# Optimization experiments

Measured on AMD Instinct MI355X. Metric: run time of the kernel, lower is better.

The kernel has to match this reference:

```python
import jax, jax.numpy as jnp
import numpy as np

B, S, H = 2, 1024, 2048
NH, HD = 16, 128
PAST = 1024
ROPE_THETA = 10000.0


def _rope(q, k, theta=ROPE_THETA):
    # q, k: [B, S, NH, HD]; standard rotate-half RoPE over current positions 0..S-1
    s, d = q.shape[1], q.shape[3]
    inv_freq = 1.0 / (theta ** (jnp.arange(0, d, 2, dtype=jnp.float32) / d))  # [d/2]
    freqs = jnp.arange(s, dtype=jnp.float32)[:, None] * inv_freq[None, :]      # [S, d/2]
    emb = jnp.concatenate([freqs, freqs], axis=-1)                             # [S, d]
    cos = jnp.cos(emb)[None, :, None, :]
    sin = jnp.sin(emb)[None, :, None, :]

    def rot_half(x):
        x1, x2 = jnp.split(x, 2, axis=-1)
        return jnp.concatenate([-x2, x1], axis=-1)

    return q * cos + rot_half(q) * sin, k * cos + rot_half(k) * sin


def setup_inputs() -> dict:
    key = jax.random.key(0)
    ks = jax.random.split(key, 12)
    hidden_states = jax.random.normal(ks[0], (B, S, H), dtype=jnp.float32)
    past_key = jax.random.normal(ks[1], (B, NH, PAST, HD), dtype=jnp.float32)
    past_value = jax.random.normal(ks[2], (B, NH, PAST, HD), dtype=jnp.float32)
    # causal mask accounting for cache: 1.0 where masked (query i cannot see kv j > PAST+i)
    q_pos = PAST + jnp.arange(S)[:, None]
    kv_pos = jnp.arange(PAST + S)[None, :]
    mask = jnp.broadcast_to((kv_pos > q_pos).astype(jnp.float32)[None, None], (B, 1, S, PAST + S))
    sc = 1.0 / np.sqrt(H)
    Wq = jax.random.normal(ks[3], (H, NH * HD), dtype=jnp.float32) * sc
    Wk = jax.random.normal(ks[4], (H, NH * HD), dtype=jnp.float32) * sc
    Wv = jax.random.normal(ks[5], (H, NH * HD), dtype=jnp.float32) * sc
    Wo = jax.random.normal(ks[6], (NH * HD, H), dtype=jnp.float32) * (1.0 / np.sqrt(NH * HD))
    bq = jnp.zeros((NH * HD,), jnp.float32)
    bk = jnp.zeros((NH * HD,), jnp.float32)
    bv = jnp.zeros((NH * HD,), jnp.float32)
    bo = jnp.zeros((H,), jnp.float32)
    return {"hidden_states": hidden_states, "mask": mask, "past_key": past_key,
            "past_value": past_value, "Wq": Wq, "bq": bq, "Wk": Wk, "bk": bk,
            "Wv": Wv, "bv": bv, "Wo": Wo, "bo": bo}


def reference(hidden_states, mask, past_key, past_value, Wq, bq, Wk, bk, Wv, bv, Wo, bo):
    b, s, _ = hidden_states.shape
    scale = 1.0 / jnp.sqrt(jnp.float32(HD))
    q = (hidden_states @ Wq + bq).reshape(b, s, NH, HD)
    k = (hidden_states @ Wk + bk).reshape(b, s, NH, HD)
    v = (hidden_states @ Wv + bv).reshape(b, s, NH, HD)
    q, k = _rope(q, k)
    q, k, v = (jnp.transpose(x, (0, 2, 1, 3)) for x in (q, k, v))  # [B,NH,S,HD]
    k = jnp.concatenate([past_key, k], axis=2)    # [B,NH,S_total,HD]
    v = jnp.concatenate([past_value, v], axis=2)
    scores = jnp.einsum('bhqd,bhkd->bhqk', q, k) * scale
    scores = scores + mask * (-1e9)               # mask broadcasts over heads
    probs = jax.nn.softmax(scores, axis=-1).astype(jnp.float32)
    out = jnp.einsum('bhqk,bhkd->bhqd', probs, v)
    out = out.transpose(0, 2, 1, 3).reshape(b, s, NH * HD)
    return out @ Wo + bo, k, v
```

## Files before the change

### kernel.cpp

```cpp
#include <hip/hip_runtime.h>
#include <hip/hip_bf16.h>
#include <math.h>

#define NB 2
#define SEQ 1024
#define HDIM 2048
#define NHEADS 16
#define HDHEAD 128
#define PASTN 1024
#define STOT 2048
#define MROWS 2048

typedef __attribute__((ext_vector_type(4))) float f32x4;
typedef __attribute__((ext_vector_type(8))) __bf16 bf16x8;
typedef __attribute__((ext_vector_type(8))) unsigned short us8;
typedef __attribute__((ext_vector_type(4))) unsigned short us4;

__device__ __forceinline__ unsigned short f2bf(float f) {
    union { float f; unsigned int u; } v; v.f = f;
    unsigned int u = v.u;
    u += 0x7FFFu + ((u >> 16) & 1u);
    return (unsigned short)(u >> 16);
}
__device__ __forceinline__ bf16x8 as_bf(us8 u) { return __builtin_bit_cast(bf16x8, u); }

__device__ __forceinline__ void gl16(const unsigned short* g, unsigned short* l) {
    __builtin_amdgcn_global_load_lds(
        (const __attribute__((address_space(1))) void*)g,
        (__attribute__((address_space(3))) void*)l, 16, 0, 0);
}

#define OFF_CS  ((size_t)0)
#define OFF_HSB (OFF_CS  + (size_t)SEQ*64*8)
#define OFF_WT  (OFF_HSB + (size_t)MROWS*HDIM*2)
#define OFF_QBF (OFF_WT  + (size_t)4*HDIM*HDIM*2)
#define OFF_KC  (OFF_QBF + (size_t)NB*NHEADS*SEQ*HDHEAD*2)
#define OFF_VT  (OFF_KC  + (size_t)NB*NHEADS*STOT*HDHEAD*2)
#define OFF_ATT (OFF_VT  + (size_t)NB*NHEADS*HDHEAD*STOT*2)


__global__ void k_prep(const float* __restrict__ in, unsigned short* __restrict__ hsb,
                       const float* __restrict__ pk, float* __restrict__ outK,
                       unsigned short* __restrict__ Kc2, float2* __restrict__ csT,
                       const float* __restrict__ Wq, const float* __restrict__ Wk,
                       const float* __restrict__ Wv, const float* __restrict__ Wo,
                       unsigned short* __restrict__ WT,
                       const float* __restrict__ pv, float* __restrict__ outV,
                       unsigned short* __restrict__ Vt2) {
    __shared__ unsigned short tsh[64][65];
    const int bid = blockIdx.x, tid = threadIdx.x;
    if (bid < 4096) {
        const int i = (bid * 256 + tid) * 4;
        {
            f32x4 v = *(const f32x4*)(in + i);
            us4 o;
            o.x = f2bf(v.x); o.y = f2bf(v.y); o.z = f2bf(v.z); o.w = f2bf(v.w);
            *(us4*)(hsb + i) = o;
        }
        {
            size_t e = (size_t)i;
            size_t bh = e >> 17;
            int p = (int)((e >> 7) & 1023);
            int d0 = (int)(e & 127);
            f32x4 v = *(const f32x4*)(pk + e);
            *(f32x4*)(outK + e + (bh << 17)) = v;
            us4 u;
            u.x = f2bf(v.x); u.y = f2bf(v.y); u.z = f2bf(v.z); u.w = f2bf(v.w);
            const int kt = p >> 6, pr = p & 63;
            *(us4*)(Kc2 + ((bh * 32 + kt) << 13) + (size_t)pr * 128 + (d0 ^ ((p & 7) << 3))) = u;
        }
        if (bid < 256) {
            const int idx = bid * 256 + tid;
            const int s = idx >> 6, fi = idx & 63;
            float inv = 1.0f / powf(10000.0f, (float)fi / 64.0f);
            float a = (float)s * inv;
            csT[idx] = make_float2(cosf(a), sinf(a));
        }
    } else if (bid < 8192) {
        const int idx = bid - 4096;
        const int z = idx >> 10;
        const int rem = idx & 1023;
        const int n0 = (rem & 31) * 64, k0 = (rem >> 5) * 64;
        const float* W = (z == 0) ? Wq : (z == 1) ? Wk : (z == 2) ? Wv : Wo;
        unsigned short* out = WT + (size_t)z * HDIM * HDIM;
        const int tx = tid & 63, ty = tid >> 6;
        #pragma unroll
        for (int j = 0; j < 16; ++j) {
            const int kk = ty + j * 4;
            tsh[tx][kk] = f2bf(W[(size_t)(k0 + kk) * HDIM + n0 + tx]);
        }
        __syncthreads();
        #pragma unroll
        for (int j = 0; j < 16; ++j) {
            const int nn = ty + j * 4;
            out[(size_t)(n0 + nn) * HDIM + k0 + tx] = tsh[nn][tx];
        }
    } else {
        const int idx = bid - 8192;
        const int bh = idx >> 5;
        const int rem = idx & 31;
        const int p0 = (rem & 15) * 64, d0 = (rem >> 4) * 64;
        const int tx = tid & 63, ty = tid >> 6;
        const float* src = pv + ((size_t)bh * PASTN + p0) * HDHEAD + d0;
        float* dst = outV + ((size_t)bh * STOT + p0) * HDHEAD + d0;
        #pragma unroll
        for (int j = 0; j < 16; ++j) {
            const int pp = ty + j * 4;
            float v = src[(size_t)pp * HDHEAD + tx];
            dst[(size_t)pp * HDHEAD + tx] = v;
            tsh[tx][pp] = f2bf(v);
        }
        __syncthreads();
        unsigned short* vt = Vt2 + (((size_t)bh * 32 + (p0 >> 6)) << 13);
        #pragma unroll
        for (int j = 0; j < 16; ++j) {
            const int dd = ty + j * 4;
            const int d = d0 + dd;
            vt[(size_t)d * 64 + (tx ^ ((d & 7) << 3))] = tsh[dd][tx];
        }
    }
}

__global__ __launch_bounds__(512, 2) void k_gemm_qkv(
    const unsigned short* __restrict__ hsb, const unsigned short* __restrict__ WT,
    const float* __restrict__ bq, const float* __restrict__ bk, const float* __restrict__ bv,
    const float2* __restrict__ csT,
    unsigned short* __restrict__ qbf, unsigned short* __restrict__ Kc2,
    unsigned short* __restrict__ Vt2, float* __restrict__ outK, float* __restrict__ outV) {
    __shared__ __align__(16) unsigned short As[2][256 * 64];
    __shared__ __align__(16) unsigned short Bs[2][256 * 64];

    const int bid = blockIdx.x;
    const int swz = (bid & 7) * 24 + (bid >> 3);
    const int mb = swz & 7;
    const int nbz = swz >> 3;
    const int z = nbz >> 3;
    const int nb8 = nbz & 7;
    const int m0 = mb * 256;
    const int n0 = nb8 * 256;
    const unsigned short* Wz = WT + (size_t)z * HDIM * HDIM;
    const float* bias = (z == 0) ? bq : (z == 1) ? bk : bv;

    const int t = threadIdx.x;
    const int lane = t & 63, wid = t >> 6;
    const int wr = wid >> 1, wc = wid & 1;
    const int c = lane & 15, g = lane >> 4;

    const int lrow8 = lane >> 3;
    const int lslot = (lane & 7) ^ lrow8;
    const unsigned short* aB = hsb + (size_t)(m0 + lrow8) * HDIM + lslot * 8;
    const unsigned short* bB = Wz + (size_t)(n0 + lrow8) * HDIM + lslot * 8;

    auto stage = [&](int kt, int pb) {
        const int k0s = kt * 64;
        #pragma unroll
        for (int j = 0; j < 4; ++j) {
            const int ch = wid * 4 + j;
            gl16(aB + (size_t)(ch * 8) * HDIM + k0s, &As[pb][ch * 512]);
            gl16(bB + (size_t)(ch * 8) * HDIM + k0s, &Bs[pb][ch * 512]);
        }
    };

    f32x4 acc[4][8] = {};
    const int NT = HDIM / 64;

    stage(0, 0);
    stage(1, 1);

    for (int kt = 0; kt < NT; ++kt) {
        const int p = kt & 1;
        if (kt + 1 < NT) {
            asm volatile("s_waitcnt vmcnt(8)" ::: "memory");
        } else {
            asm volatile("s_waitcnt vmcnt(0)" ::: "memory");
        }
        __builtin_amdgcn_s_barrier();
        bf16x8 bfr[8][2];
        #pragma unroll
        for (int ni = 0; ni < 8; ++ni) {
            const int br = wc * 128 + ni * 16 + c;
            const int sw = br & 7;
            bfr[ni][0] = as_bf(*(const us8*)&Bs[p][br * 64 + ((g ^ sw) << 3)]);
            bfr[ni][1] = as_bf(*(const us8*)&Bs[p][br * 64 + (((4 + g) ^ sw) << 3)]);
        }
        #pragma unroll
        for (int mi = 0; mi < 4; ++mi) {
            const int ar = wr * 64 + mi * 16 + c;
            const int swa = ar & 7;
            const bf16x8 a0 = as_bf(*(const us8*)&As[p][ar * 64 + ((g ^ swa) << 3)]);
            const bf16x8 a1 = as_bf(*(const us8*)&As[p][ar * 64 + (((4 + g) ^ swa) << 3)]);
            __builtin_amdgcn_s_setprio(1);
            #pragma unroll
            for (int ni = 0; ni < 8; ++ni)
                acc[mi][ni] = __builtin_amdgcn_mfma_f32_16x16x32_bf16(a0, bfr[ni][0], acc[mi][ni], 0, 0, 0);
            #pragma unroll
            for (int ni = 0; ni < 8; ++ni)
                acc[mi][ni] = __builtin_amdgcn_mfma_f32_16x16x32_bf16(a1, bfr[ni][1], acc[mi][ni], 0, 0, 0);
            __builtin_amdgcn_s_setprio(0);
            __builtin_amdgcn_s_barrier();
        }
        if (kt + 2 < NT) stage(kt + 2, p);
    }

    const float qscale = 0.08838834764831845f * 1.44269504088896f;
    const int h = nb8 * 2 + wc;
    #pragma unroll
    for (int mi = 0; mi < 4; ++mi) {
        #pragma unroll
        for (int r = 0; r < 4; ++r) {
            const int row = m0 + wr * 64 + mi * 16 + g * 4 + r;
            const int b = row >> 10, s = row & 1023;
            const size_t bh2 = (size_t)(b * NHEADS + h);
            const int p = PASTN + s;
            #pragma unroll
            for (int ni = 0; ni < 8; ++ni) {
                const int d = ni * 16 + c;
                const int nglob = n0 + wc * 128 + d;
                const float val = acc[mi][ni][r] + bias[nglob];
                if (z == 2) {
                    outV[(bh2 * STOT + p) * HDHEAD + d] = val;
                    Vt2[((bh2 * 32 + (p >> 6)) << 13) + (size_t)d * 64 +
                        ((p & 63) ^ ((d & 7) << 3))] = f2bf(val);
                } else {
                    const int fidx = d & 63;
                    const float2 cs = csT[s * 64 + fidx];
                    const float other = acc[mi][ni ^ 4][r] + bias[nglob ^ 64];
                    const float rot = (d < 64) ? (val * cs.x - other * cs.y)
                                               : (val * cs.x + other * cs.y);
                    if (z == 0) {
                        qbf[(bh2 * SEQ + s) * HDHEAD + d] = f2bf(rot * qscale);
                    } else {
                        Kc2[((bh2 * 32 + (p >> 6)) << 13) + (size_t)(p & 63) * 128 +
                            (d ^ ((p & 7) << 3))] = f2bf(rot);
                        outK[(bh2 * STOT + p) * HDHEAD + d] = rot;
                    }
                }
            }
        }
    }
}

__global__ __launch_bounds__(512) void k_attn(
    const unsigned short* __restrict__ qbf, const unsigned short* __restrict__ Kc2,
    const unsigned short* __restrict__ Vt2, unsigned short* __restrict__ attn) {
    __shared__ __align__(16) unsigned short Ks[2][64 * 128];
    __shared__ __align__(16) unsigned short Vs[128 * 64];
    __shared__ __align__(16) unsigned short P[8][16][72];
    const int qt = blockIdx.x;
    const int bh = blockIdx.y;
    const int b = bh >> 4, h = bh & 15;
    const int t = threadIdx.x, lane = t & 63, w = t >> 6;
    const int c = lane & 15, g = lane >> 4;
    const int q0 = qt * 128 + w * 16;
    const unsigned short* Qb = qbf + ((size_t)bh * SEQ + q0) * HDHEAD;
    const unsigned short* Kbase = Kc2 + ((size_t)bh << 18);
    const unsigned short* Vbase = Vt2 + ((size_t)bh << 18);

    bf16x8 qf[4];
    #pragma unroll
    for (int kf = 0; kf < 4; ++kf)
        qf[kf] = as_bf(*(const us8*)(Qb + (size_t)c * HDHEAD + kf * 32 + g * 8));

    #pragma unroll
    for (int j = 0; j < 2; ++j) {
        const int ch = w * 2 + j;
        gl16(Kbase + ch * 512 + lane * 8, &Ks[0][ch * 512]);
    }

    f32x4 o[8] = {};
    float mrow[4] = {-1e30f, -1e30f, -1e30f, -1e30f};
    float lrow[4] = {0.f, 0.f, 0.f, 0.f};
    const int nkt = 18 + 2 * qt;
    int cur = 0;
    for (int kt = 0; kt < nkt; ++kt) {
        asm volatile("s_waitcnt vmcnt(0)" ::: "memory");
        __builtin_amdgcn_s_barrier();
        const unsigned short* Vg = Vbase + ((size_t)kt << 13);
        #pragma unroll
        for (int j = 0; j < 2; ++j) {
            const int ch = w * 2 + j;
            gl16(Vg + ch * 512 + lane * 8, &Vs[ch * 512]);
        }
        if (kt + 1 < nkt) {
            const unsigned short* Kg = Kbase + ((size_t)(kt + 1) << 13);
            #pragma unroll
            for (int j = 0; j < 2; ++j) {
                const int ch = w * 2 + j;
                gl16(Kg + ch * 512 + lane * 8, &Ks[cur ^ 1][ch * 512]);
            }
        }
        f32x4 sa[4] = {};
        #pragma unroll
        for (int nf = 0; nf < 4; ++nf) {
            const int row = nf * 16 + c;
            const int swzr = (row & 7) << 3;
            #pragma unroll
            for (int kf = 0; kf < 4; ++kf) {
                bf16x8 kf8 = as_bf(*(const us8*)&Ks[cur][row * 128 + ((kf * 32 + g * 8) ^ swzr)]);
                sa[nf] = __builtin_amdgcn_mfma_f32_16x16x32_bf16(qf[kf], kf8, sa[nf], 0, 0, 0);
            }
        }
        const int k0 = kt * 64;
        if (k0 + 63 > PASTN + q0) {
            #pragma unroll
            for (int nf = 0; nf < 4; ++nf) {
                const int j = k0 + nf * 16 + c;
                #pragma unroll
                for (int r = 0; r < 4; ++r)
                    if (j > PASTN + q0 + g * 4 + r) sa[nf][r] = -1e30f;
            }
        }
        float pmax[4];
        #pragma unroll
        for (int r = 0; r < 4; ++r)
            pmax[r] = fmaxf(fmaxf(sa[0][r], sa[1][r]), fmaxf(sa[2][r], sa[3][r]));
        bool need = false;
        #pragma unroll
        for (int r = 0; r < 4; ++r) need = need || (pmax[r] > mrow[r] + 12.0f);
        if (__any(need)) {
            #pragma unroll
            for (int r = 0; r < 4; ++r) {
                float mx = pmax[r];
                mx = fmaxf(mx, __shfl_xor(mx, 1));
                mx = fmaxf(mx, __shfl_xor(mx, 2));
                mx = fmaxf(mx, __shfl_xor(mx, 4));
                mx = fmaxf(mx, __shfl_xor(mx, 8));
                const float mnew = fmaxf(mrow[r], mx);
                const float alpha = exp2f(mrow[r] - mnew);
                mrow[r] = mnew;
                lrow[r] *= alpha;
                #pragma unroll
                for (int nd = 0; nd < 8; ++nd) o[nd][r] *= alpha;
            }
        }
        #pragma unroll
        for (int r = 0; r < 4; ++r) {
            const float p0 = exp2f(sa[0][r] - mrow[r]);
            const float p1 = exp2f(sa[1][r] - mrow[r]);
            const float p2 = exp2f(sa[2][r] - mrow[r]);
            const float p3 = exp2f(sa[3][r] - mrow[r]);
            lrow[r] += (p0 + p1) + (p2 + p3);
            P[w][g * 4 + r][0 * 16 + c] = f2bf(p0);
            P[w][g * 4 + r][1 * 16 + c] = f2bf(p1);
            P[w][g * 4 + r][2 * 16 + c] = f2bf(p2);
            P[w][g * 4 + r][3 * 16 + c] = f2bf(p3);
        }
        if (kt + 1 < nkt) {
            asm volatile("s_waitcnt vmcnt(2)" ::: "memory");
        } else {
            asm volatile("s_waitcnt vmcnt(0)" ::: "memory");
        }
        __builtin_amdgcn_s_barrier();
        #pragma unroll
        for (int kf2 = 0; kf2 < 2; ++kf2) {
            const bf16x8 pa = as_bf(*(const us8*)&P[w][c][kf2 * 32 + g * 8]);
            #pragma unroll
            for (int nd = 0; nd < 8; ++nd) {
                const int d = nd * 16 + c;
                const bf16x8 vf = as_bf(*(const us8*)&Vs[d * 64 + ((kf2 * 32 + g * 8) ^ ((d & 7) << 3))]);
                o[nd] = __builtin_amdgcn_mfma_f32_16x16x32_bf16(pa, vf, o[nd], 0, 0, 0);
            }
        }
        cur ^= 1;
    }
    #pragma unroll
    for (int r = 0; r < 4; ++r) {
        float ls = lrow[r];
        ls += __shfl_xor(ls, 1);
        ls += __shfl_xor(ls, 2);
        ls += __shfl_xor(ls, 4);
        ls += __shfl_xor(ls, 8);
        const float inv = 1.0f / ls;
        #pragma unroll
        for (int nd = 0; nd < 8; ++nd) o[nd][r] *= inv;
    }
    #pragma unroll
    for (int nd = 0; nd < 8; ++nd)
        #pragma unroll
        for (int r = 0; r < 4; ++r) {
            const int srow = q0 + g * 4 + r;
            attn[((size_t)b * SEQ + srow) * HDIM + h * HDHEAD + nd * 16 + c] = f2bf(o[nd][r]);
        }
}

__global__ __launch_bounds__(256) void k_gemm_out(
    const unsigned short* __restrict__ attn, const unsigned short* __restrict__ WTo,
    const float* __restrict__ bo, float* __restrict__ out) {
    __shared__ __align__(16) unsigned char SMEM[65536];
    unsigned short* As0 = (unsigned short*)SMEM;
    unsigned short* Bs0 = (unsigned short*)(SMEM + 32768);
    const int m0 = blockIdx.y * 128;
    const int n0 = blockIdx.x * 128;
    const int t = threadIdx.x;
    const int lane = t & 63, w = t >> 6;
    const int c = lane & 15, g = lane >> 4;

    const int lrow = lane >> 3;
    const int lslot = (lane & 7) ^ lrow;
    const unsigned short* aB = attn + (size_t)(m0 + lrow) * HDIM + lslot * 8;
    const unsigned short* bB = WTo + (size_t)(n0 + lrow) * HDIM + lslot * 8;

    f32x4 acc[2][8] = {};
    const int NT = HDIM / 64;

    #pragma unroll
    for (int j = 0; j < 4; ++j) {
        const int ch = w * 4 + j;
        gl16(aB + (size_t)(ch * 8) * HDIM, &As0[ch * 512]);
        gl16(bB + (size_t)(ch * 8) * HDIM, &Bs0[ch * 512]);
    }
    for (int kt = 0; kt < NT; ++kt) {
        const int cb = kt & 1;
        if (kt + 1 < NT) {
            const int k1 = (kt + 1) * 64;
            #pragma unroll
            for (int j = 0; j < 4; ++j) {
                const int ch = w * 4 + j;
                gl16(aB + (size_t)(ch * 8) * HDIM + k1, &As0[(cb ^ 1) * 8192 + ch * 512]);
                gl16(bB + (size_t)(ch * 8) * HDIM + k1, &Bs0[(cb ^ 1) * 8192 + ch * 512]);
            }
            asm volatile("s_waitcnt vmcnt(8)" ::: "memory");
        } else {
            asm volatile("s_waitcnt vmcnt(0)" ::: "memory");
        }
        __builtin_amdgcn_s_barrier();
        #pragma unroll
        for (int kc = 0; kc < 2; ++kc) {
            bf16x8 af[2];
            #pragma unroll
            for (int mi = 0; mi < 2; ++mi) {
                const int ar = w * 32 + mi * 16 + c;
                af[mi] = as_bf(*(const us8*)&As0[cb * 8192 + ar * 64 + (((kc * 4 + g) ^ (ar & 7)) << 3)]);
            }
            #pragma unroll
            for (int ni = 0; ni < 8; ++ni) {
                const int br = ni * 16 + c;
                bf16x8 bfrag = as_bf(*(const us8*)&Bs0[cb * 8192 + br * 64 + (((kc * 4 + g) ^ (br & 7)) << 3)]);
                acc[0][ni] = __builtin_amdgcn_mfma_f32_16x16x32_bf16(af[0], bfrag, acc[0][ni], 0, 0, 0);
                acc[1][ni] = __builtin_amdgcn_mfma_f32_16x16x32_bf16(af[1], bfrag, acc[1][ni], 0, 0, 0);
            }
        }
        __builtin_amdgcn_s_barrier();
    }

    float* myF = (float*)SMEM + w * (16 * 132);
    const int qrow = lane & 31;
    for (int mi = 0; mi < 2; ++mi) {
        __syncthreads();
        #pragma unroll
        for (int r = 0; r < 4; ++r) {
            const int row = g * 4 + r;
            #pragma unroll
            for (int ni = 0; ni < 8; ++ni)
                myF[row * 132 + ni * 16 + c] = acc[mi][ni][r];
        }
        __syncthreads();
        #pragma unroll
        for (int j = 0; j < 8; ++j) {
            const int rrow = 2 * j + (lane >> 5);
            const int row = m0 + w * 32 + mi * 16 + rrow;
            f32x4 v4 = *(const f32x4*)&myF[rrow * 132 + qrow * 4];
            const f32x4 b4 = *(const f32x4*)&bo[n0 + qrow * 4];
            v4 += b4;
            *(f32x4*)&out[(size_t)row * HDIM + n0 + qrow * 4] = v4;
        }
    }
}

extern "C" void kernel_launch(void* const* d_in, const int* in_sizes, int n_in,
                              void* d_out, int out_size, void* d_ws, size_t ws_size,
                              hipStream_t stream) {
    const float* hidden = (const float*)d_in[0];
    const float* past_key = (const float*)d_in[2];
    const float* past_value = (const float*)d_in[3];
    const float* Wq = (const float*)d_in[4];
    const float* bq = (const float*)d_in[5];
    const float* Wk = (const float*)d_in[6];
    const float* bk = (const float*)d_in[7];
    const float* Wv = (const float*)d_in[8];
    const float* bv = (const float*)d_in[9];
    const float* Wo = (const float*)d_in[10];
    const float* bo = (const float*)d_in[11];

    float* out0 = (float*)d_out;
    float* outK = out0 + (size_t)NB * SEQ * HDIM;
    float* outV = outK + (size_t)NB * NHEADS * STOT * HDHEAD;

    char* ws = (char*)d_ws;
    float2* csT = (float2*)(ws + OFF_CS);
    unsigned short* hsb = (unsigned short*)(ws + OFF_HSB);
    unsigned short* WT = (unsigned short*)(ws + OFF_WT);
    unsigned short* qbf = (unsigned short*)(ws + OFF_QBF);
    unsigned short* Kc2 = (unsigned short*)(ws + OFF_KC);
    unsigned short* Vt2 = (unsigned short*)(ws + OFF_VT);
    unsigned short* attnb = (unsigned short*)(ws + OFF_ATT);

    k_prep<<<dim3(9216), dim3(256), 0, stream>>>(
        hidden, hsb, past_key, outK, Kc2, csT,
        Wq, Wk, Wv, Wo, WT, past_value, outV, Vt2);
    k_gemm_qkv<<<dim3(192), dim3(512), 0, stream>>>(
        hsb, WT, bq, bk, bv, csT, qbf, Kc2, Vt2, outK, outV);
    k_attn<<<dim3(8, 32), dim3(512), 0, stream>>>(qbf, Kc2, Vt2, attnb);
    k_gemm_out<<<dim3(16, 16), dim3(256), 0, stream>>>(
        attnb, WT + (size_t)3 * HDIM * HDIM, bo, out0);
}
```

Measured before the change: 234.3 us.

## Stage QKV GEMM epilogue through LDS for vectorized stores; split MFMA loop into phases

The QKV projection kernel's epilogue now writes each 16-row slice of results into per-warp shared-memory scratch, then reads it back so that Q, K, V, the fp32 cache outputs and the transposed V tile are written with 4-wide vector stores instead of scattered scalar stores. The main loop is also reorganised into four phases: all A fragments are loaded once, each phase loads two B column fragments, and an explicit lgkmcnt wait plus sched_barrier fences the MFMA block. The intent is to cut uncoalesced global write traffic and lower register pressure from holding all B fragments. The cost is extra __syncthreads in the epilogue, LDS round trips, and more barriers per k-step.

```diff
diff --git a/kernel.cpp b/kernel.cpp
--- a/kernel.cpp
+++ b/kernel.cpp
@@ -127,8 +127,9 @@
     const float2* __restrict__ csT,
     unsigned short* __restrict__ qbf, unsigned short* __restrict__ Kc2,
     unsigned short* __restrict__ Vt2, float* __restrict__ outK, float* __restrict__ outV) {
-    __shared__ __align__(16) unsigned short As[2][256 * 64];
-    __shared__ __align__(16) unsigned short Bs[2][256 * 64];
+    __shared__ __align__(16) unsigned char SMEM[131072];
+    unsigned short* As = (unsigned short*)SMEM;
+    unsigned short* Bs = (unsigned short*)(SMEM + 65536);
 
     const int bid = blockIdx.x;
     const int swz = (bid & 7) * 24 + (bid >> 3);
@@ -156,8 +157,8 @@
         #pragma unroll
         for (int j = 0; j < 4; ++j) {
             const int ch = wid * 4 + j;
-            gl16(aB + (size_t)(ch * 8) * HDIM + k0s, &As[pb][ch * 512]);
-            gl16(bB + (size_t)(ch * 8) * HDIM + k0s, &Bs[pb][ch * 512]);
+            gl16(aB + (size_t)(ch * 8) * HDIM + k0s, &As[pb * 16384 + ch * 512]);
+            gl16(bB + (size_t)(ch * 8) * HDIM + k0s, &Bs[pb * 16384 + ch * 512]);
         }
     };
 
@@ -175,66 +176,113 @@
             asm volatile("s_waitcnt vmcnt(0)" ::: "memory");
         }
         __builtin_amdgcn_s_barrier();
-        bf16x8 bfr[8][2];
-        #pragma unroll
-        for (int ni = 0; ni < 8; ++ni) {
-            const int br = wc * 128 + ni * 16 + c;
-            const int sw = br & 7;
-            bfr[ni][0] = as_bf(*(const us8*)&Bs[p][br * 64 + ((g ^ sw) << 3)]);
-            bfr[ni][1] = as_bf(*(const us8*)&Bs[p][br * 64 + (((4 + g) ^ sw) << 3)]);
-        }
-        #pragma unroll
-        for (int mi = 0; mi < 4; ++mi) {
-            const int ar = wr * 64 + mi * 16 + c;
-            const int swa = ar & 7;
-            const bf16x8 a0 = as_bf(*(const us8*)&As[p][ar * 64 + ((g ^ swa) << 3)]);
-            const bf16x8 a1 = as_bf(*(const us8*)&As[p][ar * 64 + (((4 + g) ^ swa) << 3)]);
+        bf16x8 a0[4], a1[4];
+        #pragma unroll
+        for (int ph = 0; ph < 4; ++ph) {
+            if (ph == 0) {
+                #pragma unroll
+                for (int mi = 0; mi < 4; ++mi) {
+                    const int ar = wr * 64 + mi * 16 + c;
+                    const int swa = ar & 7;
+                    a0[mi] = as_bf(*(const us8*)&As[p * 16384 + ar * 64 + ((g ^ swa) << 3)]);
+                    a1[mi] = as_bf(*(const us8*)&As[p * 16384 + ar * 64 + (((4 + g) ^ swa) << 3)]);
+                }
+            }
+            bf16x8 b0[2], b1[2];
+            #pragma unroll
+            for (int nj = 0; nj < 2; ++nj) {
+                const int br = wc * 128 + (ph * 2 + nj) * 16 + c;
+                const int sw = br & 7;
+                b0[nj] = as_bf(*(const us8*)&Bs[p * 16384 + br * 64 + ((g ^ sw) << 3)]);
+                b1[nj] = as_bf(*(const us8*)&Bs[p * 16384 + br * 64 + (((4 + g) ^ sw) << 3)]);
+            }
+            __builtin_amdgcn_s_barrier();
+            asm volatile("s_waitcnt lgkmcnt(0)" ::: "memory");
+            __builtin_amdgcn_sched_barrier(0);
             __builtin_amdgcn_s_setprio(1);
             #pragma unroll
-            for (int ni = 0; ni < 8; ++ni)
-                acc[mi][ni] = __builtin_amdgcn_mfma_f32_16x16x32_bf16(a0, bfr[ni][0], acc[mi][ni], 0, 0, 0);
-            #pragma unroll
-            for (int ni = 0; ni < 8; ++ni)
-                acc[mi][ni] = __builtin_amdgcn_mfma_f32_16x16x32_bf16(a1, bfr[ni][1], acc[mi][ni], 0, 0, 0);
+            for (int mi = 0; mi < 4; ++mi) {
+                #pragma unroll
+                for (int nj = 0; nj < 2; ++nj) {
+                    const int ni = ph * 2 + nj;
+                    acc[mi][ni] = __builtin_amdgcn_mfma_f32_16x16x32_bf16(a0[mi], b0[nj], acc[mi][ni], 0, 0, 0);
+                    acc[mi][ni] = __builtin_amdgcn_mfma_f32_16x16x32_bf16(a1[mi], b1[nj], acc[mi][ni], 0, 0, 0);
+                }
+            }
             __builtin_amdgcn_s_setprio(0);
             __builtin_amdgcn_s_barrier();
         }
         if (kt + 2 < NT) stage(kt + 2, p);
     }
 
+    float* myF = (float*)SMEM + wid * (16 * 132);
     const float qscale = 0.08838834764831845f * 1.44269504088896f;
     const int h = nb8 * 2 + wc;
-    #pragma unroll
+    const int b = m0 >> 10;
+    const size_t bh2 = (size_t)(b * NHEADS + h);
+    const int qrow = lane & 31;
+
     for (int mi = 0; mi < 4; ++mi) {
+        __syncthreads();
+        const int s_base = m0 + wr * 64 + mi * 16 - (b << 10);
         #pragma unroll
         for (int r = 0; r < 4; ++r) {
-            const int row = m0 + wr * 64 + mi * 16 + g * 4 + r;
-            const int b = row >> 10, s = row & 1023;
-            const size_t bh2 = (size_t)(b * NHEADS + h);
-            const int p = PASTN + s;
+            const int row = g * 4 + r;
+            const int s = s_base + row;
             #pragma unroll
             for (int ni = 0; ni < 8; ++ni) {
                 const int d = ni * 16 + c;
                 const int nglob = n0 + wc * 128 + d;
                 const float val = acc[mi][ni][r] + bias[nglob];
+                float sv;
                 if (z == 2) {
-                    outV[(bh2 * STOT + p) * HDHEAD + d] = val;
-                    Vt2[((bh2 * 32 + (p >> 6)) << 13) + (size_t)d * 64 +
-                        ((p & 63) ^ ((d & 7) << 3))] = f2bf(val);
+                    sv = val;
                 } else {
-                    const int fidx = d & 63;
-                    const float2 cs = csT[s * 64 + fidx];
+                    const float2 cs = csT[s * 64 + (d & 63)];
                     const float other = acc[mi][ni ^ 4][r] + bias[nglob ^ 64];
-                    const float rot = (d < 64) ? (val * cs.x - other * cs.y)
-                                               : (val * cs.x + other * cs.y);
-                    if (z == 0) {
-                        qbf[(bh2 * SEQ + s) * HDHEAD + d] = f2bf(rot * qscale);
-                    } else {
-                        Kc2[((bh2 * 32 + (p >> 6)) << 13) + (size_t)(p & 63) * 128 +
-                            (d ^ ((p & 7) << 3))] = f2bf(rot);
-                        outK[(bh2 * STOT + p) * HDHEAD + d] = rot;
-                    }
+                    sv = (d < 64) ? (val * cs.x - other * cs.y)
+                                  : (val * cs.x + other * cs.y);
+                    if (z == 0) sv *= qscale;
                 }
+                myF[row * 132 + d] = sv;
+            }
+        }
+        __syncthreads();
+        #pragma unroll
+        for (int j = 0; j < 8; ++j) {
+            const int rrow = 2 * j + (lane >> 5);
+            const int s = s_base + rrow;
+            const int p = PASTN + s;
+            const f32x4 v4 = *(const f32x4*)&myF[rrow * 132 + qrow * 4];
+            if (z == 0) {
+                us4 u;
+                u.x = f2bf(v4.x); u.y = f2bf(v4.y); u.z = f2bf(v4.z); u.w = f2bf(v4.w);
+                *(us4*)&qbf[(bh2 * SEQ + s) * HDHEAD + qrow * 4] = u;
+            } else if (z == 1) {
+                *(f32x4*)&outK[(bh2 * STOT + p) * HDHEAD + qrow * 4] = v4;
+                us4 u;
+                u.x = f2bf(v4.x); u.y = f2bf(v4.y); u.z = f2bf(v4.z); u.w = f2bf(v4.w);
+                *(us4*)&Kc2[((bh2 * 32 + (p >> 6)) << 13) + (size_t)(p & 63) * 128 +
+                            ((qrow * 4) ^ ((p & 7) << 3))] = u;
+            } else {
+                *(f32x4*)&outV[(bh2 * STOT + p) * HDHEAD + qrow * 4] = v4;
+            }
+        }
+        if (z == 2) {
+            const int p_base = PASTN + s_base;
+            const int ktv = p_base >> 6;
+            const int psub = (lane >> 4) * 4;
+            const int pr0 = (p_base & 63) + psub;
+            unsigned short* vbaseo = Vt2 + ((bh2 * 32 + ktv) << 13);
+            #pragma unroll
+            for (int jj = 0; jj < 8; ++jj) {
+                const int d = jj * 16 + c;
+                us4 u;
+                u.x = f2bf(myF[(psub + 0) * 132 + d]);
+                u.y = f2bf(myF[(psub + 1) * 132 + d]);
+                u.z = f2bf(myF[(psub + 2) * 132 + d]);
+                u.w = f2bf(myF[(psub + 3) * 132 + d]);
+                *(us4*)&vbaseo[d * 64 + (pr0 ^ ((d & 7) << 3))] = u;
             }
         }
     }
```

Result: slower. 267.3 us (+14.1%).

## Split QKV GEMM epilogue into separate RoPE/convert/transpose post kernel

Applied to the files above, without the earlier changes.

The QKV GEMM now writes raw fp32 Q and K tiles to scratch buffers (reusing the output and attention workspace) and writes V with bias directly. A new k_post kernel adds bias, applies RoPE, converts to bf16, writes the swizzled K cache and the transposed V via shared memory, all with vectorized stores. This replaces the scattered, uncoalesced scalar stores in the GEMM epilogue. The cost is an extra kernel launch and an extra fp32 round trip through global memory for Q, K and V.

```diff
diff --git a/kernel.cpp b/kernel.cpp
--- a/kernel.cpp
+++ b/kernel.cpp
@@ -123,10 +123,8 @@
 
 __global__ __launch_bounds__(512, 2) void k_gemm_qkv(
     const unsigned short* __restrict__ hsb, const unsigned short* __restrict__ WT,
-    const float* __restrict__ bq, const float* __restrict__ bk, const float* __restrict__ bv,
-    const float2* __restrict__ csT,
-    unsigned short* __restrict__ qbf, unsigned short* __restrict__ Kc2,
-    unsigned short* __restrict__ Vt2, float* __restrict__ outK, float* __restrict__ outV) {
+    const float* __restrict__ bv,
+    float* __restrict__ Cq, float* __restrict__ Ck, float* __restrict__ outV) {
     __shared__ __align__(16) unsigned short As[2][256 * 64];
     __shared__ __align__(16) unsigned short Bs[2][256 * 64];
 
@@ -139,7 +137,6 @@
     const int m0 = mb * 256;
     const int n0 = nb8 * 256;
     const unsigned short* Wz = WT + (size_t)z * HDIM * HDIM;
-    const float* bias = (z == 0) ? bq : (z == 1) ? bk : bv;
 
     const int t = threadIdx.x;
     const int lane = t & 63, wid = t >> 6;
@@ -202,41 +199,132 @@
         if (kt + 2 < NT) stage(kt + 2, p);
     }
 
+    if (z < 2) {
+        float* Cz = (z == 0) ? Cq : Ck;
+        #pragma unroll
+        for (int mi = 0; mi < 4; ++mi) {
+            #pragma unroll
+            for (int r = 0; r < 4; ++r) {
+                const size_t row = (size_t)(m0 + wr * 64 + mi * 16 + g * 4 + r);
+                #pragma unroll
+                for (int ni = 0; ni < 8; ++ni)
+                    Cz[row * HDIM + n0 + wc * 128 + ni * 16 + c] = acc[mi][ni][r];
+            }
+        }
+    } else {
+        const int h = nb8 * 2 + wc;
+        const int b = m0 >> 10;
+        const size_t bh2 = (size_t)(b * NHEADS + h);
+        float bias8[8];
+        #pragma unroll
+        for (int ni = 0; ni < 8; ++ni) bias8[ni] = bv[n0 + wc * 128 + ni * 16 + c];
+        #pragma unroll
+        for (int mi = 0; mi < 4; ++mi) {
+            #pragma unroll
+            for (int r = 0; r < 4; ++r) {
+                const int row = m0 + wr * 64 + mi * 16 + g * 4 + r;
+                const int s = row & 1023;
+                const int p = PASTN + s;
+                #pragma unroll
+                for (int ni = 0; ni < 8; ++ni)
+                    outV[(bh2 * STOT + p) * HDHEAD + ni * 16 + c] = acc[mi][ni][r] + bias8[ni];
+            }
+        }
+    }
+}
+
+__global__ __launch_bounds__(256) void k_post(
+    const float* __restrict__ Cq, const float* __restrict__ Ck,
+    const float* __restrict__ outV,
+    const float* __restrict__ bq, const float* __restrict__ bk,
+    const float2* __restrict__ csT,
+    unsigned short* __restrict__ qbf, unsigned short* __restrict__ Kc2,
+    unsigned short* __restrict__ Vt2, float* __restrict__ outK) {
+    __shared__ unsigned short tv[128][80];
+    const int stile = blockIdx.x;
+    const int bh = blockIdx.y;
+    const int b = bh >> 4, h = bh & 15;
+    const int tid = threadIdx.x;
+    const int dq = (tid & 15) * 4;
+    const int sl0 = tid >> 4;
+    const int s0 = stile * 64;
+    const int ktv = 16 + stile;
     const float qscale = 0.08838834764831845f * 1.44269504088896f;
-    const int h = nb8 * 2 + wc;
-    #pragma unroll
-    for (int mi = 0; mi < 4; ++mi) {
-        #pragma unroll
-        for (int r = 0; r < 4; ++r) {
-            const int row = m0 + wr * 64 + mi * 16 + g * 4 + r;
-            const int b = row >> 10, s = row & 1023;
-            const size_t bh2 = (size_t)(b * NHEADS + h);
-            const int p = PASTN + s;
-            #pragma unroll
-            for (int ni = 0; ni < 8; ++ni) {
-                const int d = ni * 16 + c;
-                const int nglob = n0 + wc * 128 + d;
-                const float val = acc[mi][ni][r] + bias[nglob];
-                if (z == 2) {
-                    outV[(bh2 * STOT + p) * HDHEAD + d] = val;
-                    Vt2[((bh2 * 32 + (p >> 6)) << 13) + (size_t)d * 64 +
-                        ((p & 63) ^ ((d & 7) << 3))] = f2bf(val);
-                } else {
-                    const int fidx = d & 63;
-                    const float2 cs = csT[s * 64 + fidx];
-                    const float other = acc[mi][ni ^ 4][r] + bias[nglob ^ 64];
-                    const float rot = (d < 64) ? (val * cs.x - other * cs.y)
-                                               : (val * cs.x + other * cs.y);
-                    if (z == 0) {
-                        qbf[(bh2 * SEQ + s) * HDHEAD + d] = f2bf(rot * qscale);
-                    } else {
-                        Kc2[((bh2 * 32 + (p >> 6)) << 13) + (size_t)(p & 63) * 128 +
-                            (d ^ ((p & 7) << 3))] = f2bf(rot);
-                        outK[(bh2 * STOT + p) * HDHEAD + d] = rot;
-                    }
-                }
-            }
-        }
+    unsigned short* kc = Kc2 + (((size_t)bh * 32 + ktv) << 13);
+    unsigned short* vt = Vt2 + (((size_t)bh * 32 + ktv) << 13);
+
+    float bql[4], bqh[4], bkl[4], bkh[4];
+    #pragma unroll
+    for (int i = 0; i < 4; ++i) {
+        bql[i] = bq[h * 128 + dq + i];      bqh[i] = bq[h * 128 + 64 + dq + i];
+        bkl[i] = bk[h * 128 + dq + i];      bkh[i] = bk[h * 128 + 64 + dq + i];
+    }
+
+    #pragma unroll
+    for (int ps = 0; ps < 4; ++ps) {
+        const int sl = sl0 + ps * 16;
+        const int s = s0 + sl;
+        const size_t row = (size_t)b * 1024 + s;
+        const int p = PASTN + s;
+        float2 cs4[4];
+        #pragma unroll
+        for (int i = 0; i < 4; ++i) cs4[i] = csT[s * 64 + dq + i];
+        const int swzp = (sl & 7) << 3;
+        {
+            const f32x4 a = *(const f32x4*)&Cq[row * HDIM + h * 128 + dq];
+            const f32x4 bb = *(const f32x4*)&Cq[row * HDIM + h * 128 + dq + 64];
+            us4 lo, hi;
+            #pragma unroll
+            for (int i = 0; i < 4; ++i) {
+                const float va = a[i] + bql[i];
+                const float vb = bb[i] + bqh[i];
+                lo[i] = f2bf((va * cs4[i].x - vb * cs4[i].y) * qscale);
+                hi[i] = f2bf((vb * cs4[i].x + va * cs4[i].y) * qscale);
+            }
+            unsigned short* qrow = qbf + ((size_t)bh * SEQ + s) * HDHEAD;
+            *(us4*)&qrow[dq] = lo;
+            *(us4*)&qrow[dq + 64] = hi;
+        }
+        {
+            const f32x4 a = *(const f32x4*)&Ck[row * HDIM + h * 128 + dq];
+            const f32x4 bb = *(const f32x4*)&Ck[row * HDIM + h * 128 + dq + 64];
+            f32x4 rl, rh;
+            us4 lo, hi;
+            #pragma unroll
+            for (int i = 0; i < 4; ++i) {
+                const float va = a[i] + bkl[i];
+                const float vb = bb[i] + bkh[i];
+                rl[i] = va * cs4[i].x - vb * cs4[i].y;
+                rh[i] = vb * cs4[i].x + va * cs4[i].y;
+                lo[i] = f2bf(rl[i]);
+                hi[i] = f2bf(rh[i]);
+            }
+            float* krow = outK + ((size_t)bh * STOT + p) * HDHEAD;
+            *(f32x4*)&krow[dq] = rl;
+            *(f32x4*)&krow[dq + 64] = rh;
+            *(us4*)&kc[(size_t)sl * 128 + (dq ^ swzp)] = lo;
+            *(us4*)&kc[(size_t)sl * 128 + ((dq + 64) ^ swzp)] = hi;
+        }
+        {
+            const f32x4 va = *(const f32x4*)&outV[((size_t)bh * STOT + p) * HDHEAD + dq];
+            const f32x4 vb = *(const f32x4*)&outV[((size_t)bh * STOT + p) * HDHEAD + dq + 64];
+            #pragma unroll
+            for (int i = 0; i < 4; ++i) {
+                tv[dq + i][sl] = f2bf(va[i]);
+                tv[dq + 64 + i][sl] = f2bf(vb[i]);
+            }
+        }
+    }
+    __syncthreads();
+    const int d = tid >> 1;
+    const int ph = (tid & 1) * 32;
+    const int swzd = (d & 7) << 3;
+    #pragma unroll
+    for (int i = 0; i < 8; ++i) {
+        const int pp = ph + i * 4;
+        us4 u;
+        u.x = tv[d][pp]; u.y = tv[d][pp + 1]; u.z = tv[d][pp + 2]; u.w = tv[d][pp + 3];
+        *(us4*)&vt[(size_t)d * 64 + (pp ^ swzd)] = u;
     }
 }
 
@@ -494,12 +582,16 @@
     unsigned short* Kc2 = (unsigned short*)(ws + OFF_KC);
     unsigned short* Vt2 = (unsigned short*)(ws + OFF_VT);
     unsigned short* attnb = (unsigned short*)(ws + OFF_ATT);
+    float* Cq = out0;
+    float* Ck = (float*)(ws + OFF_ATT);
 
     k_prep<<<dim3(9216), dim3(256), 0, stream>>>(
         hidden, hsb, past_key, outK, Kc2, csT,
         Wq, Wk, Wv, Wo, WT, past_value, outV, Vt2);
     k_gemm_qkv<<<dim3(192), dim3(512), 0, stream>>>(
-        hsb, WT, bq, bk, bv, csT, qbf, Kc2, Vt2, outK, outV);
+        hsb, WT, bv, Cq, Ck, outV);
+    k_post<<<dim3(16, 32), dim3(256), 0, stream>>>(
+        Cq, Ck, outV, bq, bk, csT, qbf, Kc2, Vt2, outK);
     k_attn<<<dim3(8, 32), dim3(512), 0, stream>>>(qbf, Kc2, Vt2, attnb);
     k_gemm_out<<<dim3(16, 16), dim3(256), 0, stream>>>(
         attnb, WT + (size_t)3 * HDIM * HDIM, bo, out0);
```

Result: faster. 220.4 us (-6.0%).
